# Performance work log

Measured on AMD Instinct MI355X. Metric: run time of the kernel, lower is better.

Reference implementation:

```python
import jax, jax.numpy as jnp
import numpy as np

EPS = 0.97  # ContrastLoss eps
T = 0.07    # temperature

def _embed(x, W, b):
    # Linear + L2 normalize (Normalize(power=2))
    h = x @ W.T + b                     # [B, feat_dim]
    norm = jnp.sqrt(jnp.sum(h * h, axis=1, keepdims=True))
    return h / norm

def setup_inputs() -> dict:
    key = jax.random.key(0)
    ks = jax.random.split(key, 7)
    B, S, Td, F = 8192, 2048, 2048, 128
    return {
        "f_s": jax.random.normal(ks[0], (B, S), jnp.float32),
        "f_t": jax.random.normal(ks[1], (B, Td), jnp.float32),
        "y": jax.random.randint(ks[2], (B,), 0, 100, jnp.int64),
        "W_s": jax.random.normal(ks[3], (F, S), jnp.float32) * 0.02,
        "b_s": jax.random.normal(ks[4], (F,), jnp.float32) * 0.02,
        "W_t": jax.random.normal(ks[5], (F, Td), jnp.float32) * 0.02,
        "b_t": jax.random.normal(ks[6], (F,), jnp.float32) * 0.02,
    }

def reference(f_s, f_t, y, W_s, b_s, W_t, b_t):
    fs = _embed(f_s, W_s, b_s)
    ft = _embed(f_t, W_t, b_t)
    # CRDLoss re-normalizes (idempotent, kept for fidelity)
    fs = fs / jnp.linalg.norm(fs, axis=1, keepdims=True)
    ft = ft / jnp.linalg.norm(ft, axis=1, keepdims=True)
    bsz = fs.shape[0]
    x = jnp.exp((fs @ ft.T) / T)  # [B, B] exponentiated similarities
    same = y[None, :] == y[:, None]        # y_expand == y_expand.T
    diag = jnp.eye(bsz, dtype=bool)
    pos_mask = same & ~diag
    neg_mask = ~same & ~diag
    # masked log-ratio sums instead of dynamic-shape gathers
    log_D1 = jnp.log(x / (x + EPS))
    log_D0 = jnp.log(EPS / (x + EPS))
    loss = -(jnp.sum(jnp.where(pos_mask, log_D1, 0.0))
             + jnp.sum(jnp.where(neg_mask, log_D0, 0.0))) / bsz
    return loss
```

## Files before the change

### kernel.cpp

```cpp
#include <hip/hip_runtime.h>
#include <math.h>


typedef _Float16 half_t;
typedef half_t halfx4 __attribute__((ext_vector_type(4)));
typedef half_t halfx8 __attribute__((ext_vector_type(8)));
typedef float f32x4 __attribute__((ext_vector_type(4)));

#define B_TOT   8192
#define K_EMB   2048
#define F_DIM   128
#define INV_T   14.285714285714286f
#define EPS_C   0.97f
#define LOG_EPS (-0.030459207485f)

__global__ __launch_bounds__(256) void embed_kernel(
    const float* __restrict__ Xs, const float* __restrict__ Xt,
    const float* __restrict__ Ws, const float* __restrict__ Wt,
    const float* __restrict__ bs, const float* __restrict__ bt,
    half_t* __restrict__ outs, half_t* __restrict__ outt)
{
    const float* X; const float* W; const float* bias; half_t* out;
    if (blockIdx.y == 0) { X = Xs; W = Ws; bias = bs; out = outs; }
    else                 { X = Xt; W = Wt; bias = bt; out = outt; }

    __shared__ half_t As[64][72];
    __shared__ half_t Bs[128][72];
    __shared__ float  biasS[128];
    __shared__ float  redS[64][2];
    __shared__ float  invS[64];

    const int tid = threadIdx.x;
    const int r0  = blockIdx.x * 64;
    if (tid < 128) biasS[tid] = bias[tid];

    const int lane = tid & 63;
    const int w    = tid >> 6;
    const int wm   = w >> 1, wn = w & 1;
    const int l16  = lane & 15, lhi = lane >> 4;

    f32x4 acc[2][4];
    for (int im = 0; im < 2; ++im)
        for (int in = 0; in < 4; ++in)
            acc[im][in] = f32x4{0.f, 0.f, 0.f, 0.f};

    for (int kb = 0; kb < K_EMB; kb += 64) {
        for (int i = 0; i < 4; ++i) {
            int f = tid + i * 256;
            int row = f >> 4, kq = f & 15;
            float4 v = *(const float4*)(X + (size_t)(r0 + row) * K_EMB + kb + kq * 4);
            halfx4 h4 = {(half_t)v.x, (half_t)v.y, (half_t)v.z, (half_t)v.w};
            *(halfx4*)&As[row][kq * 4] = h4;
        }
        for (int i = 0; i < 8; ++i) {
            int f = tid + i * 256;
            int row = f >> 4, kq = f & 15;
            float4 v = *(const float4*)(W + (size_t)row * K_EMB + kb + kq * 4);
            halfx4 h4 = {(half_t)v.x, (half_t)v.y, (half_t)v.z, (half_t)v.w};
            *(halfx4*)&Bs[row][kq * 4] = h4;
        }
        __syncthreads();
        for (int kk = 0; kk < 2; ++kk) {
            halfx8 a[2], b[4];
            for (int im = 0; im < 2; ++im)
                a[im] = *(const halfx8*)&As[wm * 32 + im * 16 + l16][kk * 32 + lhi * 8];
            for (int in = 0; in < 4; ++in)
                b[in] = *(const halfx8*)&Bs[wn * 64 + in * 16 + l16][kk * 32 + lhi * 8];
            for (int im = 0; im < 2; ++im)
                for (int in = 0; in < 4; ++in)
                    acc[im][in] = __builtin_amdgcn_mfma_f32_16x16x32_f16(
                        a[im], b[in], acc[im][in], 0, 0, 0);
        }
        __syncthreads();
    }

    float h[2][4][4];
    float psum[2][4];
    for (int im = 0; im < 2; ++im)
        for (int reg = 0; reg < 4; ++reg) {
            float p = 0.f;
            for (int in = 0; in < 4; ++in) {
                int col = wn * 64 + in * 16 + l16;
                float v = acc[im][in][reg] + biasS[col];
                h[im][in][reg] = v;
                p += v * v;
            }
            p += __shfl_xor(p, 1);
            p += __shfl_xor(p, 2);
            p += __shfl_xor(p, 4);
            p += __shfl_xor(p, 8);
            psum[im][reg] = p;
        }
    if (l16 == 0)
        for (int im = 0; im < 2; ++im)
            for (int reg = 0; reg < 4; ++reg)
                redS[wm * 32 + im * 16 + lhi * 4 + reg][wn] = psum[im][reg];
    __syncthreads();
    if (tid < 64) invS[tid] = rsqrtf(redS[tid][0] + redS[tid][1]);
    __syncthreads();

    for (int im = 0; im < 2; ++im)
        for (int in = 0; in < 4; ++in)
            for (int reg = 0; reg < 4; ++reg) {
                int row = wm * 32 + im * 16 + lhi * 4 + reg;
                int col = wn * 64 + in * 16 + l16;
                out[(size_t)(r0 + row) * F_DIM + col] =
                    (half_t)(h[im][in][reg] * invS[row]);
            }
}

__global__ __launch_bounds__(256, 2) void loss_kernel(
    const half_t* __restrict__ FS, const half_t* __restrict__ FT,
    const int* __restrict__ y, double* __restrict__ partials)
{
    __shared__ uint4 As4[128 * 16];
    __shared__ uint4 Bs4[128 * 16];

    const int tid = threadIdx.x;
    const int i0  = blockIdx.x * 128;
    const int j0  = blockIdx.y * 128;

    for (int i = 0; i < 8; ++i) {
        int f = tid + i * 256;
        int row = f >> 4, c = f & 15;
        int sw = c ^ (row & 15);
        As4[row * 16 + sw] = *(const uint4*)(FS + (size_t)(i0 + row) * F_DIM + c * 8);
        Bs4[row * 16 + sw] = *(const uint4*)(FT + (size_t)(j0 + row) * F_DIM + c * 8);
    }
    __syncthreads();

    const int lane = tid & 63;
    const int w    = tid >> 6;
    const int wm   = w >> 1, wn = w & 1;
    const int l16  = lane & 15, lhi = lane >> 4;

    f32x4 acc[4][4];
    for (int im = 0; im < 4; ++im)
        for (int in = 0; in < 4; ++in)
            acc[im][in] = f32x4{0.f, 0.f, 0.f, 0.f};

    for (int kk = 0; kk < 4; ++kk) {
        halfx8 a[4], b[4];
        for (int im = 0; im < 4; ++im) {
            int r = wm * 64 + im * 16 + l16;
            a[im] = *(const halfx8*)&As4[r * 16 + ((kk * 4 + lhi) ^ (r & 15))];
        }
        for (int in = 0; in < 4; ++in) {
            int r = wn * 64 + in * 16 + l16;
            b[in] = *(const halfx8*)&Bs4[r * 16 + ((kk * 4 + lhi) ^ (r & 15))];
        }
        for (int im = 0; im < 4; ++im)
            for (int in = 0; in < 4; ++in)
                acc[im][in] = __builtin_amdgcn_mfma_f32_16x16x32_f16(
                    a[im], b[in], acc[im][in], 0, 0, 0);
    }
    __syncthreads();

    int*   yrl  = (int*)As4;
    int*   ycl  = yrl + 128;
    float* wsum = (float*)(ycl + 128);
    if (tid < 128) yrl[tid] = y[i0 + tid];
    else           ycl[tid - 128] = y[j0 + tid - 128];
    __syncthreads();

    float local = 0.f;
    for (int im = 0; im < 4; ++im) {
        for (int reg = 0; reg < 4; ++reg) {
            int il = wm * 64 + im * 16 + lhi * 4 + reg;
            int yi = yrl[il];
            int gi = i0 + il;
            for (int in = 0; in < 4; ++in) {
                int jl = wn * 64 + in * 16 + l16;
                float s  = acc[im][in][reg];
                float sT = s * INV_T;
                float e  = __expf(sT);
                float l  = __logf(e + EPS_C);
                float term = (yi == ycl[jl]) ? (sT - l) : (LOG_EPS - l);
                if (gi != (j0 + jl)) local += term;
            }
        }
    }
    for (int m = 1; m < 64; m <<= 1) local += __shfl_xor(local, m);
    if (lane == 0) wsum[w] = local;
    __syncthreads();
    if (tid == 0)
        partials[blockIdx.y * gridDim.x + blockIdx.x] =
            ((double)wsum[0] + (double)wsum[1]) + ((double)wsum[2] + (double)wsum[3]);
}

__global__ __launch_bounds__(256) void finalize_kernel(
    const double* __restrict__ partials, float* __restrict__ out)
{
    __shared__ double sh[4];
    double loc = 0.0;
    for (int i = threadIdx.x; i < 4096; i += 256) loc += partials[i];
    for (int m = 1; m < 64; m <<= 1) loc += __shfl_xor(loc, m);
    int lane = threadIdx.x & 63, w = threadIdx.x >> 6;
    if (lane == 0) sh[w] = loc;
    __syncthreads();
    if (threadIdx.x == 0)
        out[0] = (float)(-(sh[0] + sh[1] + sh[2] + sh[3]) / (double)B_TOT);
}

extern "C" void kernel_launch(void* const* d_in, const int* in_sizes, int n_in,
                              void* d_out, int out_size, void* d_ws, size_t ws_size,
                              hipStream_t stream)
{
    const size_t WS_NEEDED = (64 << 10) + (4 << 20);
    if (ws_size < WS_NEEDED) {
        return;
    }

    const float* f_s = (const float*)d_in[0];
    const float* f_t = (const float*)d_in[1];
    const int*   y   = (const int*)d_in[2];
    const float* W_s = (const float*)d_in[3];
    const float* b_s = (const float*)d_in[4];
    const float* W_t = (const float*)d_in[5];
    const float* b_t = (const float*)d_in[6];
    float* out = (float*)d_out;

    char* ws = (char*)d_ws;
    double* partials = (double*)ws;
    half_t* fs = (half_t*)(ws + (64 << 10));
    half_t* ft = (half_t*)(ws + (64 << 10) + (2 << 20));

    embed_kernel<<<dim3(128, 2), 256, 0, stream>>>(f_s, f_t, W_s, W_t, b_s, b_t, fs, ft);
    loss_kernel<<<dim3(64, 64), 256, 0, stream>>>(fs, ft, y, partials);
    finalize_kernel<<<1, 256, 0, stream>>>(partials, out);
    (void)in_sizes; (void)n_in; (void)out_size;
}
```

Baseline: 237.2 us.

## Double-buffer embed GEMM loads and halve loss kernel shared memory footprint

The embed kernel now prefetches the next K-tile of X and W into registers while running MFMAs on the current shared-memory buffer, using two LDS buffers so there is one barrier per iteration. The aim is to hide global-load latency that was fully exposed in the serial load-sync-compute loop. The loss kernel splits the K=128 dimension into two halves staged through half-size LDS tiles and drops the occupancy hint, so more blocks can be resident. The cost is an extra mid-kernel reload with two barriers, plus higher register pressure from the prefetch registers in the embed kernel.

```diff
diff --git a/kernel.cpp b/kernel.cpp
--- a/kernel.cpp
+++ b/kernel.cpp
@@ -24,8 +24,8 @@
     if (blockIdx.y == 0) { X = Xs; W = Ws; bias = bs; out = outs; }
     else                 { X = Xt; W = Wt; bias = bt; out = outt; }
 
-    __shared__ half_t As[64][72];
-    __shared__ half_t Bs[128][72];
+    __shared__ half_t As[2][64][72];
+    __shared__ half_t Bs[2][128][72];
     __shared__ float  biasS[128];
     __shared__ float  redS[64][2];
     __shared__ float  invS[64];
@@ -44,32 +44,68 @@
         for (int in = 0; in < 4; ++in)
             acc[im][in] = f32x4{0.f, 0.f, 0.f, 0.f};
 
-    for (int kb = 0; kb < K_EMB; kb += 64) {
-        for (int i = 0; i < 4; ++i) {
-            int f = tid + i * 256;
-            int row = f >> 4, kq = f & 15;
-            float4 v = *(const float4*)(X + (size_t)(r0 + row) * K_EMB + kb + kq * 4);
-            halfx4 h4 = {(half_t)v.x, (half_t)v.y, (half_t)v.z, (half_t)v.w};
-            *(halfx4*)&As[row][kq * 4] = h4;
-        }
-        for (int i = 0; i < 8; ++i) {
-            int f = tid + i * 256;
-            int row = f >> 4, kq = f & 15;
-            float4 v = *(const float4*)(W + (size_t)row * K_EMB + kb + kq * 4);
-            halfx4 h4 = {(half_t)v.x, (half_t)v.y, (half_t)v.z, (half_t)v.w};
-            *(halfx4*)&Bs[row][kq * 4] = h4;
-        }
-        __syncthreads();
+    const int ar[4] = { (tid) >> 4, (tid + 256) >> 4, (tid + 512) >> 4, (tid + 768) >> 4 };
+    const int ak = (tid & 15) * 4;
+
+    float4 na[4], nb[8];
+
+#pragma unroll
+    for (int i = 0; i < 4; ++i)
+        na[i] = *(const float4*)(X + (size_t)(r0 + ar[i]) * K_EMB + ak);
+#pragma unroll
+    for (int i = 0; i < 8; ++i)
+        nb[i] = *(const float4*)(W + (size_t)((tid + i * 256) >> 4) * K_EMB + ak);
+#pragma unroll
+    for (int i = 0; i < 4; ++i) {
+        halfx4 h4 = {(half_t)na[i].x, (half_t)na[i].y, (half_t)na[i].z, (half_t)na[i].w};
+        *(halfx4*)&As[0][ar[i]][ak] = h4;
+    }
+#pragma unroll
+    for (int i = 0; i < 8; ++i) {
+        halfx4 h4 = {(half_t)nb[i].x, (half_t)nb[i].y, (half_t)nb[i].z, (half_t)nb[i].w};
+        *(halfx4*)&Bs[0][(tid + i * 256) >> 4][ak] = h4;
+    }
+    __syncthreads();
+
+    for (int it = 0; it < 32; ++it) {
+        const int cur = it & 1;
+        if (it < 31) {
+            const int kb = (it + 1) * 64;
+#pragma unroll
+            for (int i = 0; i < 4; ++i)
+                na[i] = *(const float4*)(X + (size_t)(r0 + ar[i]) * K_EMB + kb + ak);
+#pragma unroll
+            for (int i = 0; i < 8; ++i)
+                nb[i] = *(const float4*)(W + (size_t)((tid + i * 256) >> 4) * K_EMB + kb + ak);
+        }
+#pragma unroll
         for (int kk = 0; kk < 2; ++kk) {
             halfx8 a[2], b[4];
+#pragma unroll
             for (int im = 0; im < 2; ++im)
-                a[im] = *(const halfx8*)&As[wm * 32 + im * 16 + l16][kk * 32 + lhi * 8];
+                a[im] = *(const halfx8*)&As[cur][wm * 32 + im * 16 + l16][kk * 32 + lhi * 8];
+#pragma unroll
             for (int in = 0; in < 4; ++in)
-                b[in] = *(const halfx8*)&Bs[wn * 64 + in * 16 + l16][kk * 32 + lhi * 8];
+                b[in] = *(const halfx8*)&Bs[cur][wn * 64 + in * 16 + l16][kk * 32 + lhi * 8];
+#pragma unroll
             for (int im = 0; im < 2; ++im)
+#pragma unroll
                 for (int in = 0; in < 4; ++in)
                     acc[im][in] = __builtin_amdgcn_mfma_f32_16x16x32_f16(
                         a[im], b[in], acc[im][in], 0, 0, 0);
+        }
+        if (it < 31) {
+            const int nxt = cur ^ 1;
+#pragma unroll
+            for (int i = 0; i < 4; ++i) {
+                halfx4 h4 = {(half_t)na[i].x, (half_t)na[i].y, (half_t)na[i].z, (half_t)na[i].w};
+                *(halfx4*)&As[nxt][ar[i]][ak] = h4;
+            }
+#pragma unroll
+            for (int i = 0; i < 8; ++i) {
+                halfx4 h4 = {(half_t)nb[i].x, (half_t)nb[i].y, (half_t)nb[i].z, (half_t)nb[i].w};
+                *(halfx4*)&Bs[nxt][(tid + i * 256) >> 4][ak] = h4;
+            }
         }
         __syncthreads();
     }
@@ -109,59 +145,86 @@
             }
 }
 
-__global__ __launch_bounds__(256, 2) void loss_kernel(
+__global__ __launch_bounds__(256) void loss_kernel(
     const half_t* __restrict__ FS, const half_t* __restrict__ FT,
     const int* __restrict__ y, double* __restrict__ partials)
 {
-    __shared__ uint4 As4[128 * 16];
-    __shared__ uint4 Bs4[128 * 16];
+    __shared__ uint4 As4[128 * 8];
+    __shared__ uint4 Bs4[128 * 8];
+    __shared__ int   yrl[128], ycl[128];
+    __shared__ float wsum[4];
 
     const int tid = threadIdx.x;
     const int i0  = blockIdx.x * 128;
     const int j0  = blockIdx.y * 128;
 
-    for (int i = 0; i < 8; ++i) {
-        int f = tid + i * 256;
-        int row = f >> 4, c = f & 15;
-        int sw = c ^ (row & 15);
-        As4[row * 16 + sw] = *(const uint4*)(FS + (size_t)(i0 + row) * F_DIM + c * 8);
-        Bs4[row * 16 + sw] = *(const uint4*)(FT + (size_t)(j0 + row) * F_DIM + c * 8);
-    }
-    __syncthreads();
+    if (tid < 128) yrl[tid] = y[i0 + tid];
+    else           ycl[tid - 128] = y[j0 + tid - 128];
 
     const int lane = tid & 63;
     const int w    = tid >> 6;
     const int wm   = w >> 1, wn = w & 1;
     const int l16  = lane & 15, lhi = lane >> 4;
 
+#pragma unroll
+    for (int i = 0; i < 4; ++i) {
+        int f = tid + i * 256;
+        int row = f >> 3, c = f & 7;
+        As4[row * 8 + (c ^ (row & 7))] = *(const uint4*)(FS + (size_t)(i0 + row) * F_DIM + c * 8);
+    }
+#pragma unroll
+    for (int i = 0; i < 4; ++i) {
+        int f = tid + i * 256;
+        int row = f >> 3, c = f & 7;
+        Bs4[row * 8 + (c ^ (row & 7))] = *(const uint4*)(FT + (size_t)(j0 + row) * F_DIM + c * 8);
+    }
+    __syncthreads();
+
     f32x4 acc[4][4];
     for (int im = 0; im < 4; ++im)
         for (int in = 0; in < 4; ++in)
             acc[im][in] = f32x4{0.f, 0.f, 0.f, 0.f};
 
-    for (int kk = 0; kk < 4; ++kk) {
-        halfx8 a[4], b[4];
-        for (int im = 0; im < 4; ++im) {
-            int r = wm * 64 + im * 16 + l16;
-            a[im] = *(const halfx8*)&As4[r * 16 + ((kk * 4 + lhi) ^ (r & 15))];
-        }
-        for (int in = 0; in < 4; ++in) {
-            int r = wn * 64 + in * 16 + l16;
-            b[in] = *(const halfx8*)&Bs4[r * 16 + ((kk * 4 + lhi) ^ (r & 15))];
-        }
-        for (int im = 0; im < 4; ++im)
-            for (int in = 0; in < 4; ++in)
-                acc[im][in] = __builtin_amdgcn_mfma_f32_16x16x32_f16(
-                    a[im], b[in], acc[im][in], 0, 0, 0);
-    }
-    __syncthreads();
-
-    int*   yrl  = (int*)As4;
-    int*   ycl  = yrl + 128;
-    float* wsum = (float*)(ycl + 128);
-    if (tid < 128) yrl[tid] = y[i0 + tid];
-    else           ycl[tid - 128] = y[j0 + tid - 128];
-    __syncthreads();
+    for (int kc = 0; kc < 2; ++kc) {
+#pragma unroll
+        for (int kk = 0; kk < 2; ++kk) {
+            halfx8 a[4], b[4];
+#pragma unroll
+            for (int im = 0; im < 4; ++im) {
+                int r = wm * 64 + im * 16 + l16;
+                a[im] = *(const halfx8*)&As4[r * 8 + ((kk * 4 + lhi) ^ (r & 7))];
+            }
+#pragma unroll
+            for (int in = 0; in < 4; ++in) {
+                int r = wn * 64 + in * 16 + l16;
+                b[in] = *(const halfx8*)&Bs4[r * 8 + ((kk * 4 + lhi) ^ (r & 7))];
+            }
+#pragma unroll
+            for (int im = 0; im < 4; ++im)
+#pragma unroll
+                for (int in = 0; in < 4; ++in)
+                    acc[im][in] = __builtin_amdgcn_mfma_f32_16x16x32_f16(
+                        a[im], b[in], acc[im][in], 0, 0, 0);
+        }
+        if (kc == 0) {
+            __syncthreads();
+#pragma unroll
+            for (int i = 0; i < 4; ++i) {
+                int f = tid + i * 256;
+                int row = f >> 3, c = f & 7;
+                As4[row * 8 + (c ^ (row & 7))] =
+                    *(const uint4*)(FS + (size_t)(i0 + row) * F_DIM + 64 + c * 8);
+            }
+#pragma unroll
+            for (int i = 0; i < 4; ++i) {
+                int f = tid + i * 256;
+                int row = f >> 3, c = f & 7;
+                Bs4[row * 8 + (c ^ (row & 7))] =
+                    *(const uint4*)(FT + (size_t)(j0 + row) * F_DIM + 64 + c * 8);
+            }
+            __syncthreads();
+        }
+    }
 
     float local = 0.f;
     for (int im = 0; im < 4; ++im) {
@@ -207,9 +270,7 @@
                               hipStream_t stream)
 {
     const size_t WS_NEEDED = (64 << 10) + (4 << 20);
-    if (ws_size < WS_NEEDED) {
-        return;
-    }
+    if (ws_size < WS_NEEDED) return;
 
     const float* f_s = (const float*)d_in[0];
     const float* f_t = (const float*)d_in[1];
```

Result: faster. 215.9 us (-9.0%).
